# Optimization experiments

Hardware: AMD Instinct MI355X
Metric: run time of the kernel (lower is better)

The kernel has to match this reference:

```python
import jax, jax.numpy as jnp
import numpy as np

N_PAIRS = 100000
N_TRIP = 500000
PAIR_DIM = 128
GEOM_DIM = 4


def _mlp(x, w1, b1, w2, b2):
    return jax.nn.silu(x @ w1 + b1) @ w2 + b2


def setup_inputs() -> dict:
    key = jax.random.key(0)
    ks = jax.random.split(key, 16)

    def lin(k, fan_in, fan_out):
        bound = 1.0 / np.sqrt(fan_in)
        kw, kb = jax.random.split(k)
        w = jax.random.uniform(kw, (fan_in, fan_out), jnp.float32, -bound, bound)
        b = jax.random.uniform(kb, (fan_out,), jnp.float32, -bound, bound)
        return w, b

    psi_w1, psi_b1 = lin(ks[0], 3 * PAIR_DIM + GEOM_DIM, PAIR_DIM)
    psi_w2, psi_b2 = lin(ks[1], PAIR_DIM, PAIR_DIM)
    phi_w1, phi_b1 = lin(ks[2], 2 * PAIR_DIM, PAIR_DIM)
    phi_w2, phi_b2 = lin(ks[3], PAIR_DIM, PAIR_DIM)

    return {
        "h_pair": jax.random.normal(ks[4], (N_PAIRS, PAIR_DIM), jnp.float32),
        "pair_vu_idx": jax.random.randint(ks[5], (N_TRIP,), 0, N_PAIRS, jnp.int64 if jax.config.jax_enable_x64 else jnp.int32).astype(jnp.int32),
        "pair_uw_idx": jax.random.randint(ks[6], (N_TRIP,), 0, N_PAIRS).astype(jnp.int32),
        "pair_vw_idx": jax.random.randint(ks[7], (N_TRIP,), 0, N_PAIRS).astype(jnp.int32),
        "geom_features": jax.random.normal(ks[8], (N_TRIP, GEOM_DIM), jnp.float32),
        "psi_w1": psi_w1, "psi_b1": psi_b1, "psi_w2": psi_w2, "psi_b2": psi_b2,
        "phi_w1": phi_w1, "phi_b1": phi_b1, "phi_w2": phi_w2, "phi_b2": phi_b2,
    }


def reference(h_pair, pair_vu_idx, pair_uw_idx, pair_vw_idx, geom_features,
              psi_w1, psi_b1, psi_w2, psi_b2,
              phi_w1, phi_b1, phi_w2, phi_b2):
    # gather triplet endpoints: [T, pair_dim] each
    h_vu = h_pair[pair_vu_idx]
    h_uw = h_pair[pair_uw_idx]
    h_vw = h_pair[pair_vw_idx]
    triplet_input = jnp.concatenate([h_vu, h_uw, h_vw, geom_features], axis=-1)  # [T, 3D+G]
    m_triplet = _mlp(triplet_input, psi_w1, psi_b1, psi_w2, psi_b2)  # [T, D]
    # scatter-add back onto pairs indexed by vw
    agg = jax.ops.segment_sum(m_triplet, pair_vw_idx, num_segments=h_pair.shape[0])  # [N, D]
    updated = _mlp(jnp.concatenate([h_pair, agg], axis=-1), phi_w1, phi_b1, phi_w2, phi_b2)
    return h_pair + updated
```

## Files before the change

kernel.cpp:

```cpp
#include <hip/hip_runtime.h>
#include <hip/hip_bf16.h>

#define T_TRIP 500000
#define NP     100000
#define NTILES 7813

typedef float f32x4 __attribute__((ext_vector_type(4)));
typedef __bf16 bf16x8 __attribute__((ext_vector_type(8)));
typedef unsigned short u16;
typedef unsigned short u16x8 __attribute__((ext_vector_type(8)));

__device__ __forceinline__ u16 f2bf(float f) {
  union { float f; unsigned u; } v; v.f = f;
  unsigned r = v.u + 0x7fffu + ((v.u >> 16) & 1u);
  return (u16)(r >> 16);
}

__device__ __forceinline__ ushort4 cvt4(float4 v) {
  ushort4 o; o.x = f2bf(v.x); o.y = f2bf(v.y); o.z = f2bf(v.z); o.w = f2bf(v.w);
  return o;
}

__device__ __forceinline__ u16 cvt1_pk(float v) {
  unsigned r;
  asm("v_cvt_pk_bf16_f32 %0, %1, %1" : "=v"(r) : "v"(v));
  return (u16)r;
}

#define MFMA16(a, b, c) __builtin_amdgcn_mfma_f32_16x16x32_bf16((a), (b), (c), 0, 0, 0)

#define WAITVM(N) asm volatile("s_waitcnt vmcnt(" #N ")" ::: "memory")
#define LGKM0()   asm volatile("s_waitcnt lgkmcnt(0)" ::: "memory")

__device__ __forceinline__ void barrier_raw() {
  asm volatile("" ::: "memory");
  __builtin_amdgcn_s_barrier();
  asm volatile("" ::: "memory");
  __builtin_amdgcn_sched_barrier(0);
}

__device__ __forceinline__ void gload_lds16(const u16* g, u16* l) {
  __builtin_amdgcn_global_load_lds((const __attribute__((address_space(1))) void*)g,
                                   (__attribute__((address_space(3))) void*)l, 16, 0, 0);
}
__device__ __forceinline__ void gload_lds4(const int* g, int* l) {
  __builtin_amdgcn_global_load_lds((const __attribute__((address_space(1))) void*)g,
                                   (__attribute__((address_space(3))) void*)l, 4, 0, 0);
}

#define FP_W1A   0u
#define FP_W1B   16384u
#define FP_W1C   32768u
#define FP_W2    49152u
#define FP_PW1   65536u
#define FP_PW2   98304u
#define FP_W1D   114688u
#define FP_H     131072u
#define FP_AGG   12931072u
#define WS_NEED_BYTES 51462144ull

#define HSTR  136
#define GSTR  520
#define X2STR 264

__global__ void k_prep_fast(const float* __restrict__ psi_w1, const float* __restrict__ psi_w2,
                            const float* __restrict__ phi_w1, const float* __restrict__ phi_w2,
                            u16* __restrict__ ws) {
  int i = blockIdx.x * 256 + threadIdx.x;
  if (i < 49152) {
    int s = i / 16384, r = i % 16384;
    int n = r / 128, k = r % 128;
    ws[FP_W1A + i] = f2bf(psi_w1[(s * 128 + k) * 128 + n]);
    return;
  }
  i -= 49152;
  if (i < 16384) {
    int n = i / 128, k = i % 128;
    ws[FP_W2 + i] = f2bf(psi_w2[k * 128 + n]);
    return;
  }
  i -= 16384;
  if (i < 32768) {
    int n = i / 256, k = i % 256;
    ws[FP_PW1 + i] = f2bf(phi_w1[k * 128 + n]);
    return;
  }
  i -= 32768;
  if (i < 16384) {
    int n = i / 128, k = i % 128;
    ws[FP_PW2 + i] = f2bf(phi_w2[k * 128 + n]);
    return;
  }
  i -= 16384;
  if (i < 512) {
    int k = i / 128, n = i % 128;
    reinterpret_cast<float*>(ws + FP_W1D)[i] = psi_w1[(384 + k) * 128 + n];
  }
}

__global__ void k_hconv(const float* __restrict__ h, u16* __restrict__ H, u16* __restrict__ AGG) {
  const size_t i = (size_t)(blockIdx.x * 256 + threadIdx.x) * 8;
  float4 v0 = *reinterpret_cast<const float4*>(h + i);
  float4 v1 = *reinterpret_cast<const float4*>(h + i + 4);
  *reinterpret_cast<ushort4*>(H + i)     = cvt4(v0);
  *reinterpret_cast<ushort4*>(H + i + 4) = cvt4(v1);
  ushort4 z = {0, 0, 0, 0};
  *reinterpret_cast<ushort4*>(AGG + i)     = z;
  *reinterpret_cast<ushort4*>(AGG + i + 4) = z;
}

__global__ __launch_bounds__(256, 3) void k_triplet_fast(
    const u16* __restrict__ H,
    const int* __restrict__ ivu, const int* __restrict__ iuw, const int* __restrict__ ivw,
    const float* __restrict__ geom,
    const u16* __restrict__ W1A, const u16* __restrict__ W1B, const u16* __restrict__ W1C,
    const float* __restrict__ w1dF, const u16* __restrict__ W2T,
    const float* __restrict__ b1, const float* __restrict__ b2,
    u16* __restrict__ AGG) {
  __shared__ __align__(16) u16 XB[2][16 * GSTR];
  __shared__ __align__(16) u16 hl[64 * HSTR];
  __shared__ __align__(16) float geomF[64][4];
  __shared__ __align__(16) int aIvu[2][64];
  __shared__ __align__(16) int aIuw[64];
  __shared__ __align__(16) int svw[2][64];

  const int tid = threadIdx.x;
  const int w = tid >> 6, l = tid & 63;
  const int lr = l & 15;
  const int lk = (l >> 4) << 3;
  const int n0 = w * 32 + lr;
  const int rowh = (l >> 4) << 2;
  const int srow = l >> 4;
  const int schunk = (l & 15) ^ ((l >> 4) << 1);

  bf16x8 w2f[4][2];
#pragma unroll
  for (int ks = 0; ks < 4; ++ks)
#pragma unroll
    for (int ct = 0; ct < 2; ++ct)
      w2f[ks][ct] = *reinterpret_cast<const bf16x8*>(&W2T[(size_t)(n0 + ct * 16) * 128 + ks * 32 + lk]);
  const float b1v[2] = {b1[n0], b1[n0 + 16]};
  const float b2v[2] = {b2[n0], b2[n0 + 16]};
  float w1dv[4][2];
#pragma unroll
  for (int k = 0; k < 4; ++k) {
    w1dv[k][0] = w1dF[k * 128 + n0];
    w1dv[k][1] = w1dF[k * 128 + n0 + 16];
  }

  auto stage_src_lds = [&](const int* idxL, int buf) {
#pragma unroll
    for (int q = 0; q < 4; ++q) {
      const int g = w * 4 + q;
      const int idx = idxL[g * 4 + srow];
      gload_lds16(H + (size_t)idx * 128 + schunk * 8, &XB[buf][g * GSTR]);
    }
  };

  auto stage_aux = [&](int tn, int tn2, int buf) {
    if (w == 0) {
      int t = tn2 * 64 + l; t = (t < T_TRIP) ? t : (T_TRIP - 1);
      gload_lds4(ivu + t, &aIvu[buf][0]);
    } else if (w == 1) {
      int t = tn * 64 + l; t = (t < T_TRIP) ? t : (T_TRIP - 1);
      gload_lds4(iuw + t, &aIuw[0]);
    } else if (w == 2) {
      int t = tn * 64 + l; t = (t < T_TRIP) ? t : (T_TRIP - 1);
      gload_lds4(ivw + t, &svw[buf][0]);
    } else {
      int t = tn * 64 + l; t = (t < T_TRIP) ? t : (T_TRIP - 1);
      gload_lds16(reinterpret_cast<const u16*>(geom + (size_t)t * 4),
                  reinterpret_cast<u16*>(&geomF[0][0]));
    }
  };

  auto gemm_src = [&](const u16* WT, int buf, f32x4 (&acc)[4][2]) {
#pragma unroll
    for (int ks = 0; ks < 4; ++ks) {
      bf16x8 a[4], b[2];
#pragma unroll
      for (int rt = 0; rt < 4; ++rt) {
        const int r = rt * 16 + lr;
        const int g = r >> 2, s = r & 3;
        const int j = ks * 4 + (l >> 4);
        a[rt] = *reinterpret_cast<const bf16x8*>(&XB[buf][g * GSTR + s * 128 + ((j ^ (s << 1)) << 3)]);
      }
#pragma unroll
      for (int ct = 0; ct < 2; ++ct)
        b[ct] = *reinterpret_cast<const bf16x8*>(&WT[(size_t)(n0 + ct * 16) * 128 + ks * 32 + lk]);
#pragma unroll
      for (int rt = 0; rt < 4; ++rt)
#pragma unroll
        for (int ct = 0; ct < 2; ++ct)
          acc[rt][ct] = MFMA16(a[rt], b[ct], acc[rt][ct]);
    }
  };

  int4 dst4[4];
  f32x4 acc2c[4][2];
#pragma unroll
  for (int rt = 0; rt < 4; ++rt) {
    dst4[rt] = make_int4(-1, -1, -1, -1);
#pragma unroll
    for (int ct = 0; ct < 2; ++ct) acc2c[rt][ct] = f32x4{0.f, 0.f, 0.f, 0.f};
  }

  auto scatter_prev = [&]() {
#pragma unroll
    for (int rt = 0; rt < 4; ++rt) {
#pragma unroll
      for (int j = 0; j < 4; ++j) {
        const int dst = (&dst4[rt].x)[j];
        float v0 = acc2c[rt][0][j];
        float v1 = acc2c[rt][1][j];
        float x0 = __shfl_xor(v0, 1);
        float x1 = __shfl_xor(v1, 1);
        const bool even = (l & 1) == 0;
        float lo = even ? v0 : x1;
        float hi = even ? x0 : v1;
        const int col = even ? n0 : (n0 + 15);
        if (dst >= 0) {
          u16* p = AGG + (size_t)dst * 128 + col;
          unsigned pk;
          asm("v_cvt_pk_bf16_f32 %0, %1, %2" : "=v"(pk) : "v"(lo), "v"(hi));
          asm volatile("global_atomic_pk_add_bf16 %0, %1, off" :: "v"(p), "v"(pk) : "memory");
        }
      }
    }
  };

  int pb = 0, tb = 0;
  int tt = blockIdx.x;
  const int G = gridDim.x;

  {
    int tn2 = (tt + G < NTILES) ? tt + G : tt;
    stage_aux(tt, tn2, 0);
#pragma unroll
    for (int q = 0; q < 4; ++q) {
      const int g = w * 4 + q;
      int t = tt * 64 + g * 4 + srow; t = (t < T_TRIP) ? t : (T_TRIP - 1);
      const int idx = ivu[t];
      gload_lds16(H + (size_t)idx * 128 + schunk * 8, &XB[0][g * GSTR]);
    }
    WAITVM(0);
    barrier_raw();
  }

  for (; tt < NTILES; tt += G) {
    const int t0 = tt * 64;

    stage_src_lds(aIuw, pb ^ 1);
    WAITVM(4);
    barrier_raw();

    f32x4 acc[4][2] = {};
    gemm_src(W1A, pb, acc);
    barrier_raw();

    int4 nd[4];
#pragma unroll
    for (int rt = 0; rt < 4; ++rt)
      nd[rt] = *reinterpret_cast<const int4*>(&svw[tb][rt * 16 + rowh]);
    stage_src_lds(&svw[tb][0], pb);
    WAITVM(4);
    barrier_raw();

    gemm_src(W1B, pb ^ 1, acc);
    WAITVM(0);
    barrier_raw();

    stage_src_lds(&aIvu[tb][0], pb ^ 1);

    gemm_src(W1C, pb, acc);

    scatter_prev();

#pragma unroll
    for (int rt = 0; rt < 4; ++rt)
#pragma unroll
      for (int j = 0; j < 4; ++j) {
        const float4 g4 = *reinterpret_cast<const float4*>(&geomF[rt * 16 + rowh + j][0]);
#pragma unroll
        for (int ct = 0; ct < 2; ++ct)
          acc[rt][ct][j] += g4.x * w1dv[0][ct] + g4.y * w1dv[1][ct] +
                            g4.z * w1dv[2][ct] + g4.w * w1dv[3][ct];
      }
#pragma unroll
    for (int rt = 0; rt < 4; ++rt)
#pragma unroll
      for (int ct = 0; ct < 2; ++ct) {
        const float bb = b1v[ct];
#pragma unroll
        for (int j = 0; j < 4; ++j) {
          float v = acc[rt][ct][j] + bb;
          v = v * __builtin_amdgcn_rcpf(1.f + __expf(-v));
          hl[(rt * 16 + rowh + j) * HSTR + n0 + ct * 16] = cvt1_pk(v);
        }
      }
    LGKM0();
    barrier_raw();

    {
      int tn = (tt + G < NTILES) ? tt + G : tt;
      int tn2 = (tt + 2 * G < NTILES) ? tt + 2 * G : tt;
      stage_aux(tn, tn2, tb ^ 1);
    }

    f32x4 acc2[4][2] = {};
#pragma unroll
    for (int ks = 0; ks < 4; ++ks) {
      bf16x8 a[4];
#pragma unroll
      for (int rt = 0; rt < 4; ++rt)
        a[rt] = *reinterpret_cast<const bf16x8*>(&hl[(rt * 16 + lr) * HSTR + ks * 32 + lk]);
#pragma unroll
      for (int rt = 0; rt < 4; ++rt)
#pragma unroll
        for (int ct = 0; ct < 2; ++ct)
          acc2[rt][ct] = MFMA16(a[rt], w2f[ks][ct], acc2[rt][ct]);
    }

#pragma unroll
    for (int rt = 0; rt < 4; ++rt) {
#pragma unroll
      for (int j = 0; j < 4; ++j) {
        const int trow = t0 + rt * 16 + rowh + j;
        (&dst4[rt].x)[j] = (trow < T_TRIP) ? (&nd[rt].x)[j] : -1;
      }
#pragma unroll
      for (int ct = 0; ct < 2; ++ct)
        acc2c[rt][ct] = acc2[rt][ct] + b2v[ct];
    }

    WAITVM(0);
    barrier_raw();
    pb ^= 1; tb ^= 1;
  }

  scatter_prev();
  WAITVM(0);
}

__global__ __launch_bounds__(256, 3) void k_pair_fast(
    const float* __restrict__ h_pair, const u16* __restrict__ H, const u16* __restrict__ AGG,
    const u16* __restrict__ PW1T, const u16* __restrict__ PW2T,
    const float* __restrict__ b1, const float* __restrict__ b2,
    float* __restrict__ out) {
  __shared__ __align__(16) u16 xl[64 * X2STR];
  __shared__ __align__(16) u16 hl[64 * HSTR];

  const int tid = threadIdx.x;
  const int r0 = blockIdx.x * 64;

  {
    const int row = tid >> 2, q = tid & 3;
    int rc = r0 + row; rc = (rc < NP) ? rc : (NP - 1);
    const u16x8* sh = reinterpret_cast<const u16x8*>(H + (size_t)rc * 128 + q * 32);
    const u16x8* sa = reinterpret_cast<const u16x8*>(AGG + (size_t)rc * 128 + q * 32);
    u16x8* d1 = reinterpret_cast<u16x8*>(&xl[row * X2STR + q * 32]);
    u16x8* d2 = reinterpret_cast<u16x8*>(&xl[row * X2STR + 128 + q * 32]);
#pragma unroll
    for (int i = 0; i < 4; ++i) { d1[i] = sh[i]; d2[i] = sa[i]; }
  }
  __syncthreads();

  const int w = tid >> 6, l = tid & 63;
  const int lr = l & 15;
  const int lk = (l >> 4) << 3;
  const int n0 = w * 32 + lr;
  const int rowh = (l >> 4) << 2;

  f32x4 acc[4][2] = {};
#pragma unroll 1
  for (int ks = 0; ks < 8; ++ks) {
    const int k0 = ks * 32;
    bf16x8 a[4], b[2];
#pragma unroll
    for (int rt = 0; rt < 4; ++rt)
      a[rt] = *reinterpret_cast<const bf16x8*>(&xl[(rt * 16 + lr) * X2STR + k0 + lk]);
#pragma unroll
    for (int ct = 0; ct < 2; ++ct)
      b[ct] = *reinterpret_cast<const bf16x8*>(&PW1T[(size_t)(n0 + ct * 16) * 256 + k0 + lk]);
#pragma unroll
    for (int rt = 0; rt < 4; ++rt)
#pragma unroll
      for (int ct = 0; ct < 2; ++ct)
        acc[rt][ct] = MFMA16(a[rt], b[ct], acc[rt][ct]);
  }

  {
    const float b1v0 = b1[n0], b1v1 = b1[n0 + 16];
#pragma unroll
    for (int rt = 0; rt < 4; ++rt)
#pragma unroll
      for (int ct = 0; ct < 2; ++ct) {
        const float bb = ct ? b1v1 : b1v0;
#pragma unroll
        for (int j = 0; j < 4; ++j) {
          float v = acc[rt][ct][j] + bb;
          v = v * __builtin_amdgcn_rcpf(1.f + __expf(-v));
          hl[(rt * 16 + rowh + j) * HSTR + n0 + ct * 16] = cvt1_pk(v);
        }
      }
  }
  __syncthreads();

  f32x4 acc2[4][2] = {};
#pragma unroll
  for (int ks = 0; ks < 4; ++ks) {
    const int k0 = ks * 32;
    bf16x8 a[4], b[2];
#pragma unroll
    for (int rt = 0; rt < 4; ++rt)
      a[rt] = *reinterpret_cast<const bf16x8*>(&hl[(rt * 16 + lr) * HSTR + k0 + lk]);
#pragma unroll
    for (int ct = 0; ct < 2; ++ct)
      b[ct] = *reinterpret_cast<const bf16x8*>(&PW2T[(size_t)(n0 + ct * 16) * 128 + k0 + lk]);
#pragma unroll
    for (int rt = 0; rt < 4; ++rt)
#pragma unroll
      for (int ct = 0; ct < 2; ++ct)
        acc2[rt][ct] = MFMA16(a[rt], b[ct], acc2[rt][ct]);
  }

  {
    const float b2v0 = b2[n0], b2v1 = b2[n0 + 16];
#pragma unroll
    for (int rt = 0; rt < 4; ++rt)
#pragma unroll
      for (int j = 0; j < 4; ++j) {
        const int row = rt * 16 + rowh + j;
        const int r = r0 + row;
        if (r < NP) {
          out[(size_t)r * 128 + n0]      = h_pair[(size_t)r * 128 + n0]      + acc2[rt][0][j] + b2v0;
          out[(size_t)r * 128 + n0 + 16] = h_pair[(size_t)r * 128 + n0 + 16] + acc2[rt][1][j] + b2v1;
        }
      }
  }
}

#define PSI_W1T_OFF 0
#define PSI_W2T_OFF 53248
#define PHI_W1T_OFF 69632
#define PHI_W2T_OFF 102400
#define WS_U16_TOTAL 118784
#define XSTR 424

__global__ void k_prep(const float* __restrict__ psi_w1, const float* __restrict__ psi_w2,
                       const float* __restrict__ phi_w1, const float* __restrict__ phi_w2,
                       u16* __restrict__ ws) {
  int i = blockIdx.x * 256 + threadIdx.x;
  if (i < 128 * 416) {
    int n = i / 416, k = i % 416;
    ws[PSI_W1T_OFF + i] = f2bf(k < 388 ? psi_w1[k * 128 + n] : 0.f);
    return;
  }
  i -= 128 * 416;
  if (i < 128 * 128) {
    int n = i / 128, k = i % 128;
    ws[PSI_W2T_OFF + i] = f2bf(psi_w2[k * 128 + n]);
    return;
  }
  i -= 128 * 128;
  if (i < 128 * 256) {
    int n = i / 256, k = i % 256;
    ws[PHI_W1T_OFF + i] = f2bf(phi_w1[k * 128 + n]);
    return;
  }
  i -= 128 * 256;
  if (i < 128 * 128) {
    int n = i / 128, k = i % 128;
    ws[PHI_W2T_OFF + i] = f2bf(phi_w2[k * 128 + n]);
  }
}

__global__ __launch_bounds__(256, 2) void k_triplet(
    const float* __restrict__ h_pair,
    const int* __restrict__ ivu, const int* __restrict__ iuw, const int* __restrict__ ivw,
    const float* __restrict__ geom,
    const u16* __restrict__ W1T, const u16* __restrict__ W2T,
    const float* __restrict__ b1, const float* __restrict__ b2,
    float* __restrict__ agg) {
  __shared__ __align__(16) u16 xl[64 * XSTR];
  __shared__ __align__(16) u16 hl[64 * HSTR];
  __shared__ int svw[64];

  const int tid = threadIdx.x;
  const int t0 = blockIdx.x * 64;

  {
    const int row = tid >> 2, q = tid & 3;
    const int t = t0 + row;
    const int tc = (t < T_TRIP) ? t : (T_TRIP - 1);
    if (q == 0) svw[row] = (t < T_TRIP) ? ivw[tc] : -1;
    int idx[3];
    idx[0] = ivu[tc]; idx[1] = iuw[tc]; idx[2] = ivw[tc];
#pragma unroll
    for (int s = 0; s < 3; ++s) {
      const float4* src = reinterpret_cast<const float4*>(h_pair + (size_t)idx[s] * 128 + q * 32);
      u16* dst = &xl[row * XSTR + s * 128 + q * 32];
#pragma unroll
      for (int i = 0; i < 8; ++i)
        *reinterpret_cast<ushort4*>(dst + i * 4) = cvt4(src[i]);
    }
  }
  if (tid < 64) {
    const int t = t0 + tid;
    const int tc = (t < T_TRIP) ? t : (T_TRIP - 1);
    const float4 g = reinterpret_cast<const float4*>(geom)[tc];
    u16* dst = &xl[tid * XSTR + 384];
    *reinterpret_cast<ushort4*>(dst) = cvt4(g);
    ushort4 z = {0, 0, 0, 0};
#pragma unroll
    for (int i = 1; i < 8; ++i) *reinterpret_cast<ushort4*>(dst + i * 4) = z;
  }
  __syncthreads();

  const int w = tid >> 6;
  const int l = tid & 63;
  const int lr = l & 15;
  const int lk = (l >> 4) << 3;
  const int n0 = w * 32 + lr;
  const int rowh = (l >> 4) << 2;

  f32x4 acc[4][2] = {};
#pragma unroll 1
  for (int ks = 0; ks < 13; ++ks) {
    const int k0 = ks * 32;
    bf16x8 a[4], b[2];
#pragma unroll
    for (int rt = 0; rt < 4; ++rt)
      a[rt] = *reinterpret_cast<const bf16x8*>(&xl[(rt * 16 + lr) * XSTR + k0 + lk]);
#pragma unroll
    for (int ct = 0; ct < 2; ++ct)
      b[ct] = *reinterpret_cast<const bf16x8*>(&W1T[(size_t)(n0 + ct * 16) * 416 + k0 + lk]);
#pragma unroll
    for (int rt = 0; rt < 4; ++rt)
#pragma unroll
      for (int ct = 0; ct < 2; ++ct)
        acc[rt][ct] = MFMA16(a[rt], b[ct], acc[rt][ct]);
  }

  {
    const float b1v0 = b1[n0], b1v1 = b1[n0 + 16];
#pragma unroll
    for (int rt = 0; rt < 4; ++rt)
#pragma unroll
      for (int ct = 0; ct < 2; ++ct) {
        const float bb = ct ? b1v1 : b1v0;
#pragma unroll
        for (int j = 0; j < 4; ++j) {
          float v = acc[rt][ct][j] + bb;
          v = v / (1.f + __expf(-v));
          hl[(rt * 16 + rowh + j) * HSTR + n0 + ct * 16] = f2bf(v);
        }
      }
  }
  __syncthreads();

  f32x4 acc2[4][2] = {};
#pragma unroll
  for (int ks = 0; ks < 4; ++ks) {
    const int k0 = ks * 32;
    bf16x8 a[4], b[2];
#pragma unroll
    for (int rt = 0; rt < 4; ++rt)
      a[rt] = *reinterpret_cast<const bf16x8*>(&hl[(rt * 16 + lr) * HSTR + k0 + lk]);
#pragma unroll
    for (int ct = 0; ct < 2; ++ct)
      b[ct] = *reinterpret_cast<const bf16x8*>(&W2T[(size_t)(n0 + ct * 16) * 128 + k0 + lk]);
#pragma unroll
    for (int rt = 0; rt < 4; ++rt)
#pragma unroll
      for (int ct = 0; ct < 2; ++ct)
        acc2[rt][ct] = MFMA16(a[rt], b[ct], acc2[rt][ct]);
  }

  {
    const float b2v0 = b2[n0], b2v1 = b2[n0 + 16];
#pragma unroll
    for (int rt = 0; rt < 4; ++rt)
#pragma unroll
      for (int j = 0; j < 4; ++j) {
        const int row = rt * 16 + rowh + j;
        const int dst = svw[row];
        if (dst >= 0) {
          unsafeAtomicAdd(&agg[(size_t)dst * 128 + n0], acc2[rt][0][j] + b2v0);
          unsafeAtomicAdd(&agg[(size_t)dst * 128 + n0 + 16], acc2[rt][1][j] + b2v1);
        }
      }
  }
}

__global__ __launch_bounds__(256, 2) void k_pair(
    const float* __restrict__ h_pair,
    const u16* __restrict__ W1T, const u16* __restrict__ W2T,
    const float* __restrict__ b1, const float* __restrict__ b2,
    float* __restrict__ out) {
  __shared__ __align__(16) u16 xl[64 * X2STR];
  __shared__ __align__(16) u16 hl[64 * HSTR];

  const int tid = threadIdx.x;
  const int r0 = blockIdx.x * 64;

  {
    const int row = tid >> 2, q = tid & 3;
    const int r = r0 + row;
    const int rc = (r < NP) ? r : (NP - 1);
    const float4* s1 = reinterpret_cast<const float4*>(h_pair + (size_t)rc * 128 + q * 32);
    const float4* s2 = reinterpret_cast<const float4*>(out + (size_t)rc * 128 + q * 32);
    u16* d1 = &xl[row * X2STR + q * 32];
    u16* d2 = &xl[row * X2STR + 128 + q * 32];
#pragma unroll
    for (int i = 0; i < 8; ++i) {
      *reinterpret_cast<ushort4*>(d1 + i * 4) = cvt4(s1[i]);
      *reinterpret_cast<ushort4*>(d2 + i * 4) = cvt4(s2[i]);
    }
  }
  __syncthreads();

  const int w = tid >> 6;
  const int l = tid & 63;
  const int lr = l & 15;
  const int lk = (l >> 4) << 3;
  const int n0 = w * 32 + lr;
  const int rowh = (l >> 4) << 2;

  f32x4 acc[4][2] = {};
#pragma unroll 1
  for (int ks = 0; ks < 8; ++ks) {
    const int k0 = ks * 32;
    bf16x8 a[4], b[2];
#pragma unroll
    for (int rt = 0; rt < 4; ++rt)
      a[rt] = *reinterpret_cast<const bf16x8*>(&xl[(rt * 16 + lr) * X2STR + k0 + lk]);
#pragma unroll
    for (int ct = 0; ct < 2; ++ct)
      b[ct] = *reinterpret_cast<const bf16x8*>(&W1T[(size_t)(n0 + ct * 16) * 256 + k0 + lk]);
#pragma unroll
    for (int rt = 0; rt < 4; ++rt)
#pragma unroll
      for (int ct = 0; ct < 2; ++ct)
        acc[rt][ct] = MFMA16(a[rt], b[ct], acc[rt][ct]);
  }

  {
    const float b1v0 = b1[n0], b1v1 = b1[n0 + 16];
#pragma unroll
    for (int rt = 0; rt < 4; ++rt)
#pragma unroll
      for (int ct = 0; ct < 2; ++ct) {
        const float bb = ct ? b1v1 : b1v0;
#pragma unroll
        for (int j = 0; j < 4; ++j) {
          float v = acc[rt][ct][j] + bb;
          v = v / (1.f + __expf(-v));
          hl[(rt * 16 + rowh + j) * HSTR + n0 + ct * 16] = f2bf(v);
        }
      }
  }
  __syncthreads();

  f32x4 acc2[4][2] = {};
#pragma unroll
  for (int ks = 0; ks < 4; ++ks) {
    const int k0 = ks * 32;
    bf16x8 a[4], b[2];
#pragma unroll
    for (int rt = 0; rt < 4; ++rt)
      a[rt] = *reinterpret_cast<const bf16x8*>(&hl[(rt * 16 + lr) * HSTR + k0 + lk]);
#pragma unroll
    for (int ct = 0; ct < 2; ++ct)
      b[ct] = *reinterpret_cast<const bf16x8*>(&W2T[(size_t)(n0 + ct * 16) * 128 + k0 + lk]);
#pragma unroll
    for (int rt = 0; rt < 4; ++rt)
#pragma unroll
      for (int ct = 0; ct < 2; ++ct)
        acc2[rt][ct] = MFMA16(a[rt], b[ct], acc2[rt][ct]);
  }

  {
    const float b2v0 = b2[n0], b2v1 = b2[n0 + 16];
#pragma unroll
    for (int rt = 0; rt < 4; ++rt)
#pragma unroll
      for (int j = 0; j < 4; ++j) {
        const int row = rt * 16 + rowh + j;
        const int r = r0 + row;
        if (r < NP) {
          out[(size_t)r * 128 + n0]      = h_pair[(size_t)r * 128 + n0]      + acc2[rt][0][j] + b2v0;
          out[(size_t)r * 128 + n0 + 16] = h_pair[(size_t)r * 128 + n0 + 16] + acc2[rt][1][j] + b2v1;
        }
      }
  }
}

extern "C" void kernel_launch(void* const* d_in, const int* in_sizes, int n_in,
                              void* d_out, int out_size, void* d_ws, size_t ws_size,
                              hipStream_t stream) {
  const float* h_pair = (const float*)d_in[0];
  const int* ivu = (const int*)d_in[1];
  const int* iuw = (const int*)d_in[2];
  const int* ivw = (const int*)d_in[3];
  const float* geom = (const float*)d_in[4];
  const float* psi_w1 = (const float*)d_in[5];
  const float* psi_b1 = (const float*)d_in[6];
  const float* psi_w2 = (const float*)d_in[7];
  const float* psi_b2 = (const float*)d_in[8];
  const float* phi_w1 = (const float*)d_in[9];
  const float* phi_b1 = (const float*)d_in[10];
  const float* phi_w2 = (const float*)d_in[11];
  const float* phi_b2 = (const float*)d_in[12];

  float* out = (float*)d_out;
  u16* ws = (u16*)d_ws;

  if (ws_size >= WS_NEED_BYTES) {
    k_prep_fast<<<450, 256, 0, stream>>>(psi_w1, psi_w2, phi_w1, phi_w2, ws);
    k_hconv<<<6250, 256, 0, stream>>>(h_pair, ws + FP_H, ws + FP_AGG);
    k_triplet_fast<<<768, 256, 0, stream>>>(
        ws + FP_H, ivu, iuw, ivw, geom,
        ws + FP_W1A, ws + FP_W1B, ws + FP_W1C,
        reinterpret_cast<const float*>(ws + FP_W1D), ws + FP_W2,
        psi_b1, psi_b2, ws + FP_AGG);
    k_pair_fast<<<(NP + 63) / 64, 256, 0, stream>>>(
        h_pair, ws + FP_H, ws + FP_AGG,
        ws + FP_PW1, ws + FP_PW2, phi_b1, phi_b2, out);
  } else {
    hipMemsetAsync(d_out, 0, (size_t)out_size * sizeof(float), stream);
    k_prep<<<(WS_U16_TOTAL + 255) / 256, 256, 0, stream>>>(psi_w1, psi_w2, phi_w1, phi_w2, ws);
    k_triplet<<<(T_TRIP + 63) / 64, 256, 0, stream>>>(
        h_pair, ivu, iuw, ivw, geom,
        ws + PSI_W1T_OFF, ws + PSI_W2T_OFF, psi_b1, psi_b2, out);
    k_pair<<<(NP + 63) / 64, 256, 0, stream>>>(
        h_pair, ws + PHI_W1T_OFF, ws + PHI_W2T_OFF, phi_b1, phi_b2, out);
  }
}
```

Baseline: 299.3 us.

## Sort triplets by destination pair and pre-reduce segments before atomic scatter

Adds a counting-sort pass (histogram, three-stage scan, permutation) that reorders triplets by pair_vw index into a packed AoS buffer holding indices and geometry. The triplet kernel then reads this buffer, stages the MLP output through LDS, and sums consecutive rows that share a destination before issuing one bf16 atomic per run. This cuts scattered atomic traffic and index/geom loads. The cost is several extra kernel launches, atomics for the histogram and cursor, a 16 MB permuted write, and the loss of the earlier overlap between the scatter and the next tile's compute. The weight-prep and h-conversion kernels are also merged into a single launch.

```diff
diff --git a/kernel.cpp b/kernel.cpp
--- a/kernel.cpp
+++ b/kernel.cpp
@@ -4,11 +4,13 @@
 #define T_TRIP 500000
 #define NP     100000
 #define NTILES 7813
+#define NPAD   500032
 
 typedef float f32x4 __attribute__((ext_vector_type(4)));
 typedef __bf16 bf16x8 __attribute__((ext_vector_type(8)));
 typedef unsigned short u16;
 typedef unsigned short u16x8 __attribute__((ext_vector_type(8)));
+typedef unsigned int u32;
 
 __device__ __forceinline__ u16 f2bf(float f) {
   union { float f; unsigned u; } v; v.f = f;
@@ -25,6 +27,13 @@
   unsigned r;
   asm("v_cvt_pk_bf16_f32 %0, %1, %1" : "=v"(r) : "v"(v));
   return (u16)r;
+}
+
+__device__ __forceinline__ float bflo(u32 d) {
+  union { u32 u; float f; } v; v.u = d << 16; return v.f;
+}
+__device__ __forceinline__ float bfhi(u32 d) {
+  union { u32 u; float f; } v; v.u = d & 0xffff0000u; return v.f;
 }
 
 #define MFMA16(a, b, c) __builtin_amdgcn_mfma_f32_16x16x32_bf16((a), (b), (c), 0, 0, 0)
@@ -57,72 +66,146 @@
 #define FP_W1D   114688u
 #define FP_H     131072u
 #define FP_AGG   12931072u
-#define WS_NEED_BYTES 51462144ull
-
-#define HSTR  136
-#define GSTR  520
-#define X2STR 264
-
-__global__ void k_prep_fast(const float* __restrict__ psi_w1, const float* __restrict__ psi_w2,
-                            const float* __restrict__ phi_w1, const float* __restrict__ phi_w2,
-                            u16* __restrict__ ws) {
+#define SB_CNT2    51462144ull
+#define SB_CURSOR2 51862144ull
+#define SB_BSUM2   52262144ull
+#define SB_TRIP    52262656ull
+#define WS_S2      68263680ull
+
+#define HSTR   136
+#define HSTR2  132
+#define GSTR   520
+#define X2STR  264
+
+__global__ void k_pre(const float* __restrict__ psi_w1, const float* __restrict__ psi_w2,
+                      const float* __restrict__ phi_w1, const float* __restrict__ phi_w2,
+                      const float* __restrict__ h, const int* __restrict__ ivw,
+                      u16* __restrict__ ws, int* __restrict__ cnt) {
+  const int b = blockIdx.x;
+  if (b < 450) {
+    int i = b * 256 + threadIdx.x;
+    if (i < 49152) {
+      int s = i / 16384, r = i % 16384;
+      int n = r / 128, k = r % 128;
+      ws[FP_W1A + i] = f2bf(psi_w1[(s * 128 + k) * 128 + n]);
+      return;
+    }
+    i -= 49152;
+    if (i < 16384) {
+      int n = i / 128, k = i % 128;
+      ws[FP_W2 + i] = f2bf(psi_w2[k * 128 + n]);
+      return;
+    }
+    i -= 16384;
+    if (i < 32768) {
+      int n = i / 256, k = i % 256;
+      ws[FP_PW1 + i] = f2bf(phi_w1[k * 128 + n]);
+      return;
+    }
+    i -= 32768;
+    if (i < 16384) {
+      int n = i / 128, k = i % 128;
+      ws[FP_PW2 + i] = f2bf(phi_w2[k * 128 + n]);
+      return;
+    }
+    i -= 16384;
+    if (i < 512) {
+      int k = i / 128, n = i % 128;
+      reinterpret_cast<float*>(ws + FP_W1D)[i] = psi_w1[(384 + k) * 128 + n];
+    }
+  } else if (b < 6700) {
+    const size_t i = (size_t)((b - 450) * 256 + threadIdx.x) * 8;
+    float4 v0 = *reinterpret_cast<const float4*>(h + i);
+    float4 v1 = *reinterpret_cast<const float4*>(h + i + 4);
+    *reinterpret_cast<ushort4*>(ws + FP_H + i)     = cvt4(v0);
+    *reinterpret_cast<ushort4*>(ws + FP_H + i + 4) = cvt4(v1);
+    ushort4 z = {0, 0, 0, 0};
+    *reinterpret_cast<ushort4*>(ws + FP_AGG + i)     = z;
+    *reinterpret_cast<ushort4*>(ws + FP_AGG + i + 4) = z;
+  } else {
+    int i = (b - 6700) * 256 + threadIdx.x;
+    if (i < T_TRIP) atomicAdd(&cnt[ivw[i]], 1);
+  }
+}
+
+__global__ __launch_bounds__(1024) void k_scan1(const int* __restrict__ cnt,
+                                                int* __restrict__ cursor, int* __restrict__ bsum) {
+  __shared__ int wsum[16];
+  const int idx = blockIdx.x * 1024 + threadIdx.x;
+  const int lane = threadIdx.x & 63, wid = threadIdx.x >> 6;
+  int v = (idx < NP) ? cnt[idx] : 0;
+  int x = v;
+#pragma unroll
+  for (int off = 1; off < 64; off <<= 1) {
+    int n = __shfl_up(x, off);
+    if (lane >= off) x += n;
+  }
+  if (lane == 63) wsum[wid] = x;
+  __syncthreads();
+  if (threadIdx.x < 16) {
+    int s = wsum[threadIdx.x];
+#pragma unroll
+    for (int off = 1; off < 16; off <<= 1) {
+      int n = __shfl_up(s, off);
+      if (threadIdx.x >= off) s += n;
+    }
+    wsum[threadIdx.x] = s;
+  }
+  __syncthreads();
+  const int base = wid ? wsum[wid - 1] : 0;
+  if (idx < NP) cursor[idx] = base + x - v;
+  if (threadIdx.x == 1023) bsum[blockIdx.x] = base + x;
+}
+
+__global__ void k_scan2(int* __restrict__ bsum) {
+  __shared__ int s[128];
+  const int t = threadIdx.x;
+  int v = (t < 98) ? bsum[t] : 0;
+  s[t] = v; __syncthreads();
+#pragma unroll
+  for (int off = 1; off < 128; off <<= 1) {
+    int a = (t >= off) ? s[t - off] : 0;
+    __syncthreads();
+    s[t] += a;
+    __syncthreads();
+  }
+  if (t < 98) bsum[t] = s[t] - v;
+}
+
+__global__ void k_scan3(const int* __restrict__ bsum, int* __restrict__ cursor) {
+  int idx = blockIdx.x * 256 + threadIdx.x;
+  if (idx < NP) cursor[idx] += bsum[idx >> 10];
+}
+
+__global__ void k_perm_aos(const int* __restrict__ ivu, const int* __restrict__ iuw,
+                           const int* __restrict__ ivw, const float* __restrict__ geom,
+                           int* __restrict__ cursor, int4* __restrict__ trip) {
   int i = blockIdx.x * 256 + threadIdx.x;
-  if (i < 49152) {
-    int s = i / 16384, r = i % 16384;
-    int n = r / 128, k = r % 128;
-    ws[FP_W1A + i] = f2bf(psi_w1[(s * 128 + k) * 128 + n]);
-    return;
-  }
-  i -= 49152;
-  if (i < 16384) {
-    int n = i / 128, k = i % 128;
-    ws[FP_W2 + i] = f2bf(psi_w2[k * 128 + n]);
-    return;
-  }
-  i -= 16384;
-  if (i < 32768) {
-    int n = i / 256, k = i % 256;
-    ws[FP_PW1 + i] = f2bf(phi_w1[k * 128 + n]);
-    return;
-  }
-  i -= 32768;
-  if (i < 16384) {
-    int n = i / 128, k = i % 128;
-    ws[FP_PW2 + i] = f2bf(phi_w2[k * 128 + n]);
-    return;
-  }
-  i -= 16384;
-  if (i < 512) {
-    int k = i / 128, n = i % 128;
-    reinterpret_cast<float*>(ws + FP_W1D)[i] = psi_w1[(384 + k) * 128 + n];
-  }
-}
-
-__global__ void k_hconv(const float* __restrict__ h, u16* __restrict__ H, u16* __restrict__ AGG) {
-  const size_t i = (size_t)(blockIdx.x * 256 + threadIdx.x) * 8;
-  float4 v0 = *reinterpret_cast<const float4*>(h + i);
-  float4 v1 = *reinterpret_cast<const float4*>(h + i + 4);
-  *reinterpret_cast<ushort4*>(H + i)     = cvt4(v0);
-  *reinterpret_cast<ushort4*>(H + i + 4) = cvt4(v1);
-  ushort4 z = {0, 0, 0, 0};
-  *reinterpret_cast<ushort4*>(AGG + i)     = z;
-  *reinterpret_cast<ushort4*>(AGG + i + 4) = z;
-}
-
-__global__ __launch_bounds__(256, 3) void k_triplet_fast(
-    const u16* __restrict__ H,
-    const int* __restrict__ ivu, const int* __restrict__ iuw, const int* __restrict__ ivw,
-    const float* __restrict__ geom,
+  if (i < T_TRIP) {
+    int v = ivw[i];
+    int pos = atomicAdd(&cursor[v], 1);
+    int4 hdr; hdr.x = ivu[i]; hdr.y = iuw[i]; hdr.z = v; hdr.w = 0;
+    float4 g = reinterpret_cast<const float4*>(geom)[i];
+    trip[(size_t)pos * 2] = hdr;
+    reinterpret_cast<float4*>(trip)[(size_t)pos * 2 + 1] = g;
+  } else if (i < NPAD) {
+    int4 z = {0, 0, 0, 0};
+    trip[(size_t)i * 2] = z;
+    trip[(size_t)i * 2 + 1] = z;
+  }
+}
+
+__global__ __launch_bounds__(256, 3) void k_triplet_sortagg(
+    const u16* __restrict__ H, const int* __restrict__ trip,
     const u16* __restrict__ W1A, const u16* __restrict__ W1B, const u16* __restrict__ W1C,
     const float* __restrict__ w1dF, const u16* __restrict__ W2T,
     const float* __restrict__ b1, const float* __restrict__ b2,
     u16* __restrict__ AGG) {
   __shared__ __align__(16) u16 XB[2][16 * GSTR];
-  __shared__ __align__(16) u16 hl[64 * HSTR];
-  __shared__ __align__(16) float geomF[64][4];
-  __shared__ __align__(16) int aIvu[2][64];
-  __shared__ __align__(16) int aIuw[64];
-  __shared__ __align__(16) int svw[2][64];
+  __shared__ __align__(16) u16 hl[64 * HSTR2];
+  __shared__ __align__(16) int aosT[2][512];
+
+  u32* mlu = reinterpret_cast<u32*>(hl);
 
   const int tid = threadIdx.x;
   const int w = tid >> 6, l = tid & 63;
@@ -148,30 +231,19 @@
     w1dv[k][1] = w1dF[k * 128 + n0 + 16];
   }
 
-  auto stage_src_lds = [&](const int* idxL, int buf) {
+  auto stage_src = [&](int cb, int sel, int buf) {
 #pragma unroll
     for (int q = 0; q < 4; ++q) {
       const int g = w * 4 + q;
-      const int idx = idxL[g * 4 + srow];
+      const int idx = aosT[cb][(g * 4 + srow) * 8 + sel];
       gload_lds16(H + (size_t)idx * 128 + schunk * 8, &XB[buf][g * GSTR]);
     }
   };
 
-  auto stage_aux = [&](int tn, int tn2, int buf) {
-    if (w == 0) {
-      int t = tn2 * 64 + l; t = (t < T_TRIP) ? t : (T_TRIP - 1);
-      gload_lds4(ivu + t, &aIvu[buf][0]);
-    } else if (w == 1) {
-      int t = tn * 64 + l; t = (t < T_TRIP) ? t : (T_TRIP - 1);
-      gload_lds4(iuw + t, &aIuw[0]);
-    } else if (w == 2) {
-      int t = tn * 64 + l; t = (t < T_TRIP) ? t : (T_TRIP - 1);
-      gload_lds4(ivw + t, &svw[buf][0]);
-    } else {
-      int t = tn * 64 + l; t = (t < T_TRIP) ? t : (T_TRIP - 1);
-      gload_lds16(reinterpret_cast<const u16*>(geom + (size_t)t * 4),
-                  reinterpret_cast<u16*>(&geomF[0][0]));
-    }
+  auto stage_aos = [&](int tile, int cb) {
+    const int* src = trip + (size_t)tile * 512;
+    gload_lds4(src + w * 64 + l,       &aosT[cb][w * 64]);
+    gload_lds4(src + 256 + w * 64 + l, &aosT[cb][256 + w * 64]);
   };
 
   auto gemm_src = [&](const u16* WT, int buf, f32x4 (&acc)[4][2]) {
@@ -196,149 +268,131 @@
     }
   };
 
-  int4 dst4[4];
-  f32x4 acc2c[4][2];
-#pragma unroll
-  for (int rt = 0; rt < 4; ++rt) {
-    dst4[rt] = make_int4(-1, -1, -1, -1);
-#pragma unroll
-    for (int ct = 0; ct < 2; ++ct) acc2c[rt][ct] = f32x4{0.f, 0.f, 0.f, 0.f};
-  }
-
-  auto scatter_prev = [&]() {
-#pragma unroll
-    for (int rt = 0; rt < 4; ++rt) {
+  int cur = 0, pb = 0;
+  int tt = blockIdx.x;
+  const int G = gridDim.x;
+
+  {
+    int t1 = tt + G; if (t1 >= NTILES) t1 = NTILES - 1;
+    stage_aos(tt, 0);
+    stage_aos(t1, 1);
+    WAITVM(0);
+    barrier_raw();
+    stage_src(0, 0 , 0);
+  }
+
+  for (; tt < NTILES; tt += G) {
+    const int t0 = tt * 64;
+
+    stage_src(cur, 1 , pb ^ 1);
+    WAITVM(4);
+    barrier_raw();
+
+    f32x4 acc[4][2] = {};
+    gemm_src(W1A, pb, acc);
+    barrier_raw();
+
+    stage_src(cur, 2 , pb);
+    WAITVM(4);
+    barrier_raw();
+
+    gemm_src(W1B, pb ^ 1, acc);
+    WAITVM(0);
+    barrier_raw();
+
+    stage_src(cur ^ 1, 0 , pb ^ 1);
+    gemm_src(W1C, pb, acc);
+
+#pragma unroll
+    for (int rt = 0; rt < 4; ++rt)
 #pragma unroll
       for (int j = 0; j < 4; ++j) {
-        const int dst = (&dst4[rt].x)[j];
-        float v0 = acc2c[rt][0][j];
-        float v1 = acc2c[rt][1][j];
+        const int row = rt * 16 + rowh + j;
+        const float4 g4 = *reinterpret_cast<const float4*>(&aosT[cur][row * 8 + 4]);
+#pragma unroll
+        for (int ct = 0; ct < 2; ++ct)
+          acc[rt][ct][j] += g4.x * w1dv[0][ct] + g4.y * w1dv[1][ct] +
+                            g4.z * w1dv[2][ct] + g4.w * w1dv[3][ct];
+      }
+#pragma unroll
+    for (int rt = 0; rt < 4; ++rt)
+#pragma unroll
+      for (int ct = 0; ct < 2; ++ct) {
+        const float bb = b1v[ct];
+#pragma unroll
+        for (int j = 0; j < 4; ++j) {
+          float v = acc[rt][ct][j] + bb;
+          v = v * __builtin_amdgcn_rcpf(1.f + __expf(-v));
+          hl[(rt * 16 + rowh + j) * HSTR2 + n0 + ct * 16] = cvt1_pk(v);
+        }
+      }
+    LGKM0();
+    barrier_raw();
+
+    f32x4 acc2[4][2] = {};
+#pragma unroll
+    for (int ks = 0; ks < 4; ++ks) {
+      bf16x8 a[4];
+#pragma unroll
+      for (int rt = 0; rt < 4; ++rt)
+        a[rt] = *reinterpret_cast<const bf16x8*>(&hl[(rt * 16 + lr) * HSTR2 + ks * 32 + lk]);
+#pragma unroll
+      for (int rt = 0; rt < 4; ++rt)
+#pragma unroll
+        for (int ct = 0; ct < 2; ++ct)
+          acc2[rt][ct] = MFMA16(a[rt], w2f[ks][ct], acc2[rt][ct]);
+    }
+    barrier_raw();
+
+#pragma unroll
+    for (int rt = 0; rt < 4; ++rt)
+#pragma unroll
+      for (int j = 0; j < 4; ++j) {
+        const int row = rt * 16 + rowh + j;
+        float v0 = acc2[rt][0][j] + b2v[0];
+        float v1 = acc2[rt][1][j] + b2v[1];
         float x0 = __shfl_xor(v0, 1);
         float x1 = __shfl_xor(v1, 1);
         const bool even = (l & 1) == 0;
         float lo = even ? v0 : x1;
         float hi = even ? x0 : v1;
-        const int col = even ? n0 : (n0 + 15);
-        if (dst >= 0) {
-          u16* p = AGG + (size_t)dst * 128 + col;
-          unsigned pk;
+        const int dcol = even ? (n0 >> 1) : ((n0 + 15) >> 1);
+        u32 pk;
+        asm("v_cvt_pk_bf16_f32 %0, %1, %2" : "=v"(pk) : "v"(lo), "v"(hi));
+        mlu[row * 66 + dcol] = pk;
+      }
+    LGKM0();
+    barrier_raw();
+
+    {
+      float lo = 0.f, hi = 0.f;
+      int vwc = aosT[cur][(w * 16) * 8 + 2];
+#pragma unroll 1
+      for (int r8 = 0; r8 < 16; ++r8) {
+        const int row = w * 16 + r8;
+        const u32 d = mlu[row * 66 + l];
+        if (t0 + row < T_TRIP) { lo += bflo(d); hi += bfhi(d); }
+        const int vwn = (row < 63) ? aosT[cur][(row + 1) * 8 + 2] : -1;
+        if ((r8 == 15) || (vwn != vwc)) {
+          u16* p = AGG + (size_t)vwc * 128 + l * 2;
+          u32 pk;
           asm("v_cvt_pk_bf16_f32 %0, %1, %2" : "=v"(pk) : "v"(lo), "v"(hi));
           asm volatile("global_atomic_pk_add_bf16 %0, %1, off" :: "v"(p), "v"(pk) : "memory");
+          lo = 0.f; hi = 0.f; vwc = vwn;
         }
       }
     }
-  };
-
-  int pb = 0, tb = 0;
-  int tt = blockIdx.x;
-  const int G = gridDim.x;
-
-  {
-    int tn2 = (tt + G < NTILES) ? tt + G : tt;
-    stage_aux(tt, tn2, 0);
-#pragma unroll
-    for (int q = 0; q < 4; ++q) {
-      const int g = w * 4 + q;
-      int t = tt * 64 + g * 4 + srow; t = (t < T_TRIP) ? t : (T_TRIP - 1);
-      const int idx = ivu[t];
-      gload_lds16(H + (size_t)idx * 128 + schunk * 8, &XB[0][g * GSTR]);
-    }
+    barrier_raw();
+
+    {
+      int t2 = tt + 2 * G; if (t2 >= NTILES) t2 = NTILES - 1;
+      stage_aos(t2, cur);
+    }
+
     WAITVM(0);
     barrier_raw();
-  }
-
-  for (; tt < NTILES; tt += G) {
-    const int t0 = tt * 64;
-
-    stage_src_lds(aIuw, pb ^ 1);
-    WAITVM(4);
-    barrier_raw();
-
-    f32x4 acc[4][2] = {};
-    gemm_src(W1A, pb, acc);
-    barrier_raw();
-
-    int4 nd[4];
-#pragma unroll
-    for (int rt = 0; rt < 4; ++rt)
-      nd[rt] = *reinterpret_cast<const int4*>(&svw[tb][rt * 16 + rowh]);
-    stage_src_lds(&svw[tb][0], pb);
-    WAITVM(4);
-    barrier_raw();
-
-    gemm_src(W1B, pb ^ 1, acc);
-    WAITVM(0);
-    barrier_raw();
-
-    stage_src_lds(&aIvu[tb][0], pb ^ 1);
-
-    gemm_src(W1C, pb, acc);
-
-    scatter_prev();
-
-#pragma unroll
-    for (int rt = 0; rt < 4; ++rt)
-#pragma unroll
-      for (int j = 0; j < 4; ++j) {
-        const float4 g4 = *reinterpret_cast<const float4*>(&geomF[rt * 16 + rowh + j][0]);
-#pragma unroll
-        for (int ct = 0; ct < 2; ++ct)
-          acc[rt][ct][j] += g4.x * w1dv[0][ct] + g4.y * w1dv[1][ct] +
-                            g4.z * w1dv[2][ct] + g4.w * w1dv[3][ct];
-      }
-#pragma unroll
-    for (int rt = 0; rt < 4; ++rt)
-#pragma unroll
-      for (int ct = 0; ct < 2; ++ct) {
-        const float bb = b1v[ct];
-#pragma unroll
-        for (int j = 0; j < 4; ++j) {
-          float v = acc[rt][ct][j] + bb;
-          v = v * __builtin_amdgcn_rcpf(1.f + __expf(-v));
-          hl[(rt * 16 + rowh + j) * HSTR + n0 + ct * 16] = cvt1_pk(v);
-        }
-      }
-    LGKM0();
-    barrier_raw();
-
-    {
-      int tn = (tt + G < NTILES) ? tt + G : tt;
-      int tn2 = (tt + 2 * G < NTILES) ? tt + 2 * G : tt;
-      stage_aux(tn, tn2, tb ^ 1);
-    }
-
-    f32x4 acc2[4][2] = {};
-#pragma unroll
-    for (int ks = 0; ks < 4; ++ks) {
-      bf16x8 a[4];
-#pragma unroll
-      for (int rt = 0; rt < 4; ++rt)
-        a[rt] = *reinterpret_cast<const bf16x8*>(&hl[(rt * 16 + lr) * HSTR + ks * 32 + lk]);
-#pragma unroll
-      for (int rt = 0; rt < 4; ++rt)
-#pragma unroll
-        for (int ct = 0; ct < 2; ++ct)
-          acc2[rt][ct] = MFMA16(a[rt], w2f[ks][ct], acc2[rt][ct]);
-    }
-
-#pragma unroll
-    for (int rt = 0; rt < 4; ++rt) {
-#pragma unroll
-      for (int j = 0; j < 4; ++j) {
-        const int trow = t0 + rt * 16 + rowh + j;
-        (&dst4[rt].x)[j] = (trow < T_TRIP) ? (&nd[rt].x)[j] : -1;
-      }
-#pragma unroll
-      for (int ct = 0; ct < 2; ++ct)
-        acc2c[rt][ct] = acc2[rt][ct] + b2v[ct];
-    }
-
-    WAITVM(0);
-    barrier_raw();
-    pb ^= 1; tb ^= 1;
-  }
-
-  scatter_prev();
+    pb ^= 1; cur ^= 1;
+  }
   WAITVM(0);
 }
 
@@ -715,12 +769,22 @@
 
   float* out = (float*)d_out;
   u16* ws = (u16*)d_ws;
-
-  if (ws_size >= WS_NEED_BYTES) {
-    k_prep_fast<<<450, 256, 0, stream>>>(psi_w1, psi_w2, phi_w1, phi_w2, ws);
-    k_hconv<<<6250, 256, 0, stream>>>(h_pair, ws + FP_H, ws + FP_AGG);
-    k_triplet_fast<<<768, 256, 0, stream>>>(
-        ws + FP_H, ivu, iuw, ivw, geom,
+  char* wsb = (char*)d_ws;
+
+  if (ws_size >= WS_S2) {
+    int*  cnt    = (int*)(wsb + SB_CNT2);
+    int*  cursor = (int*)(wsb + SB_CURSOR2);
+    int*  bsum   = (int*)(wsb + SB_BSUM2);
+    int4* trip   = (int4*)(wsb + SB_TRIP);
+
+    hipMemsetAsync(cnt, 0, NP * sizeof(int), stream);
+    k_pre<<<8654, 256, 0, stream>>>(psi_w1, psi_w2, phi_w1, phi_w2, h_pair, ivw, ws, cnt);
+    k_scan1<<<98, 1024, 0, stream>>>(cnt, cursor, bsum);
+    k_scan2<<<1, 128, 0, stream>>>(bsum);
+    k_scan3<<<391, 256, 0, stream>>>(bsum, cursor);
+    k_perm_aos<<<(NPAD + 255) / 256, 256, 0, stream>>>(ivu, iuw, ivw, geom, cursor, trip);
+    k_triplet_sortagg<<<768, 256, 0, stream>>>(
+        ws + FP_H, (const int*)trip,
         ws + FP_W1A, ws + FP_W1B, ws + FP_W1C,
         reinterpret_cast<const float*>(ws + FP_W1D), ws + FP_W2,
         psi_b1, psi_b2, ws + FP_AGG);
```

New measurement: 376.3 us. 1.26x slower.
